# Kernel tuning notes

Measured on AMD Instinct MI355X. Metric: run time of the kernel, lower is better.

The kernel has to match this reference:

```python
import jax, jax.numpy as jnp
import numpy as np

VOCAB = 50257
W_DIM = 1024   # embedding / input width (config.n_embd)
H_DIM = 1024   # LSTM hidden size
NUM_CLASSES = 2
B, T = 32, 2048


def setup_inputs() -> dict:
    key = jax.random.key(0)
    ks = jax.random.split(key, 7)
    s = 0.02
    seq = jax.random.randint(ks[0], (B, T), 0, VOCAB)
    emb = jax.random.normal(ks[1], (VOCAB, W_DIM), dtype=jnp.float32) * s
    W_ih = jax.random.normal(ks[2], (4 * H_DIM, W_DIM), dtype=jnp.float32) * s
    W_hh = jax.random.normal(ks[3], (4 * H_DIM, H_DIM), dtype=jnp.float32) * s
    b_ih = jax.random.normal(ks[4], (4 * H_DIM,), dtype=jnp.float32) * s
    b_hh = jax.random.normal(ks[5], (4 * H_DIM,), dtype=jnp.float32) * s
    W_score = jax.random.normal(ks[6], (NUM_CLASSES, H_DIM), dtype=jnp.float32) * s
    return {"seq": seq, "emb": emb, "W_ih": W_ih, "W_hh": W_hh,
            "b_ih": b_ih, "b_hh": b_hh, "W_score": W_score}


def _lstm_scan(x_gates, W_hh):
    # x_gates: [T, B, 4H] = precomputed input contribution + biases
    H = W_hh.shape[1]
    h0 = jnp.zeros((x_gates.shape[1], H), dtype=x_gates.dtype)
    c0 = jnp.zeros_like(h0)

    def step(carry, xg):
        h, c = carry
        gates = xg + h @ W_hh.T                 # [B, 4H]
        i, f, g, o = jnp.split(gates, 4, axis=-1)  # PyTorch LSTMCell gate order
        i = jax.nn.sigmoid(i)
        f = jax.nn.sigmoid(f)
        g = jnp.tanh(g)
        o = jax.nn.sigmoid(o)
        c = f * c + i * g
        h = o * jnp.tanh(c)
        return (h, c), h

    _, hs = jax.lax.scan(step, (h0, c0), x_gates)  # hs: [T, B, H]
    return hs


def reference(seq, emb, W_ih, W_hh, b_ih, b_hh, W_score):
    # fudge=True: return per-timestep logits [B, T, num_classes]. Dropout in eval mode (identity).
    x = emb[seq]                                      # [B, T, W]
    x_gates = jnp.einsum('btw,gw->btg', x, W_ih) + b_ih + b_hh  # [B, T, 4H]
    hs = _lstm_scan(x_gates.transpose(1, 0, 2), W_hh)           # [T, B, H]
    h = hs.transpose(1, 0, 2)                         # [B, T, H]
    out = jnp.maximum(h, 0.0) @ W_score.T             # score_net: ReLU -> Linear(no bias)
    return out
```

## Files before the change

### kernel.cpp

```cpp
#include <hip/hip_runtime.h>
#include <hip/hip_bf16.h>


typedef _Float16 f16;
typedef _Float16 f16x8 __attribute__((ext_vector_type(8)));
typedef _Float16 f16x4 __attribute__((ext_vector_type(4)));
typedef float    f32x4 __attribute__((ext_vector_type(4)));
typedef unsigned long long u64;

#define B_    32
#define T_    2048
#define H_    1024
#define G4_   4096

__device__ __forceinline__ void gl_lds16(const void* g, void* l) {
  __builtin_amdgcn_global_load_lds(
      (const __attribute__((address_space(1))) void*)g,
      (__attribute__((address_space(3))) void*)l, 16, 0, 0);
}

__device__ __forceinline__ void llc_st64(void* p, u64 v) {
  __hip_atomic_store((u64*)p, v, __ATOMIC_RELAXED, __HIP_MEMORY_SCOPE_AGENT);
}

__device__ __forceinline__ float fast_sigmoid(float v) {
  return __builtin_amdgcn_rcpf(1.f + __expf(-v));
}
__device__ __forceinline__ float fast_tanh(float v) {
  return 1.f - 2.f * __builtin_amdgcn_rcpf(1.f + __expf(2.f * v));
}


__global__ void k_cvt_f16(const float* __restrict__ in, f16* __restrict__ out, long n4) {
  long i = (long)blockIdx.x * blockDim.x + threadIdx.x;
  if (i >= n4) return;
  float4 v = ((const float4*)in)[i];
  f16x4 o; o[0] = (f16)v.x; o[1] = (f16)v.y; o[2] = (f16)v.z; o[3] = (f16)v.w;
  *(f16x4*)(out + i * 4) = o;
}

__global__ void k_whh_reorder(const float* __restrict__ whh, f16* __restrict__ wr) {
  unsigned i = blockIdx.x * blockDim.x + threadIdx.x;
  unsigned e0 = i * 8;
  unsigned R = e0 >> 10, k = e0 & 1023;
  unsigned q = R >> 10, j = R & 1023;
  unsigned outR = ((j >> 4) << 6) + ((j & 15) << 2) + q;
  float4 v0 = ((const float4*)whh)[e0 / 4];
  float4 v1 = ((const float4*)whh)[e0 / 4 + 1];
  f16x8 o;
  o[0] = (f16)v0.x; o[1] = (f16)v0.y; o[2] = (f16)v0.z; o[3] = (f16)v0.w;
  o[4] = (f16)v1.x; o[5] = (f16)v1.y; o[6] = (f16)v1.z; o[7] = (f16)v1.w;
  *(f16x8*)&wr[((size_t)outR << 10) + k] = o;
}

__global__ void k_bias(const float* __restrict__ bi, const float* __restrict__ bh,
                       float* __restrict__ bo) {
  unsigned i = blockIdx.x * blockDim.x + threadIdx.x;
  if (i < G4_) bo[i] = bi[i] + bh[i];
}


__global__ __launch_bounds__(256) void k_gemm_xg(
    const int* __restrict__ seq, const f16* __restrict__ emb16,
    const f16* __restrict__ wih16, const float* __restrict__ bias,
    f16* __restrict__ xg) {
  __shared__ f16 As[128 * 64];
  __shared__ f16 Bs[128 * 64];
  const unsigned tid = threadIdx.x;
  const unsigned w = tid >> 6, lane = tid & 63;
  const unsigned bid = blockIdx.x;
  const unsigned tn = bid & 31, tm = bid >> 5;
  const unsigned wm = (w >> 1) * 64, wn = (w & 1) * 64;

  f32x4 zero = {0.f, 0.f, 0.f, 0.f};
  f32x4 acc[4][4];
#pragma unroll
  for (int i = 0; i < 4; ++i)
#pragma unroll
    for (int j = 0; j < 4; ++j) acc[i][j] = zero;

  for (unsigned kk = 0; kk < 16; ++kk) {
    const unsigned k0 = kk * 64;
#pragma unroll
    for (unsigned c = 0; c < 4; ++c) {
      unsigned idx = c * 256 + tid;
      unsigned row = idx >> 3, ch = idx & 7;
      unsigned chs = ch ^ (row & 7);
      unsigned m = tm * 128 + row;
      unsigned t = m >> 5, b = m & 31;
      int e = seq[b * 2048 + t];
      const f16* src = emb16 + ((size_t)e << 10) + k0 + chs * 8;
      gl_lds16(src, (char*)As + c * 4096 + w * 1024);
    }
#pragma unroll
    for (unsigned c = 0; c < 4; ++c) {
      unsigned idx = c * 256 + tid;
      unsigned row = idx >> 3, ch = idx & 7;
      unsigned chs = ch ^ (row & 7);
      unsigned n = tn * 128 + row;
      const f16* src = wih16 + ((size_t)n << 10) + k0 + chs * 8;
      gl_lds16(src, (char*)Bs + c * 4096 + w * 1024);
    }
    __syncthreads();
#pragma unroll
    for (unsigned ks = 0; ks < 2; ++ks) {
      f16x8 af[4], bf[4];
      unsigned kc = ks * 4 + (lane >> 4);
#pragma unroll
      for (unsigned fm = 0; fm < 4; ++fm) {
        unsigned r = wm + fm * 16 + (lane & 15);
        af[fm] = *(const f16x8*)&As[r * 64 + ((kc ^ (r & 7)) << 3)];
      }
#pragma unroll
      for (unsigned fn = 0; fn < 4; ++fn) {
        unsigned r = wn + fn * 16 + (lane & 15);
        bf[fn] = *(const f16x8*)&Bs[r * 64 + ((kc ^ (r & 7)) << 3)];
      }
#pragma unroll
      for (unsigned fm = 0; fm < 4; ++fm)
#pragma unroll
        for (unsigned fn = 0; fn < 4; ++fn)
          acc[fm][fn] = __builtin_amdgcn_mfma_f32_16x16x32_f16(af[fm], bf[fn], acc[fm][fn], 0, 0, 0);
    }
    __syncthreads();
  }
#pragma unroll
  for (unsigned fn = 0; fn < 4; ++fn) {
    unsigned n = tn * 128 + wn + fn * 16 + (lane & 15);
    unsigned q = n >> 10, j = n & 1023;
    unsigned Rp = ((j >> 4) << 6) + ((j & 15) << 2) + q;
    float bv = bias[n];
#pragma unroll
    for (unsigned fm = 0; fm < 4; ++fm) {
#pragma unroll
      for (unsigned rg = 0; rg < 4; ++rg) {
        unsigned m = tm * 128 + wm + fm * 16 + (lane >> 4) * 4 + rg;
        xg[(size_t)m * G4_ + Rp] = (f16)(acc[fm][fn][rg] + bv);
      }
    }
  }
}


__global__ __launch_bounds__(256) void k_lstm(
    const f16* __restrict__ xg, const f16* __restrict__ wr16,
    f16* __restrict__ h_all) {
  __shared__ f16 Wl[64 * 512];
  __shared__ f16 Hl[2][16 * 1024];
  const unsigned tid = threadIdx.x;
  const unsigned nt = tid >> 6, lane = tid & 63;
  const unsigned wid = blockIdx.x;
  const unsigned rl = lane & 15, hi = lane >> 4;

  for (unsigned c = 0; c < 16; ++c) {
    unsigned idx = c * 256 + tid;
    unsigned row = idx >> 6, ch = idx & 63;
    unsigned chs = ch ^ (row & 7);
    const f16* src = wr16 + (((size_t)wid * 64 + row) << 10) + chs * 8;
    gl_lds16(src, (char*)Wl + c * 4096 + nt * 1024);
  }

  const unsigned rWl = nt * 16 + rl;
  f16x8 breg[16];
  {
    const f16* wp = wr16 + (((size_t)wid * 64 + rWl) << 10) + 512 + hi * 8;
#pragma unroll
    for (int j = 0; j < 16; ++j) {
      asm volatile("global_load_dwordx4 %0, %1, off\n\ts_waitcnt vmcnt(0)"
                   : "=v"(breg[j]) : "v"(wp + j * 32) : "memory");
    }
  }
  __syncthreads();

  const unsigned srow = tid >> 4;
  const unsigned scg = (tid & 15) * 8;
  float cA = 0.f, cB = 0.f;

  for (unsigned t = 1; t <= (unsigned)T_; ++t) {
#pragma unroll
    for (int s = 0; s < 2; ++s) {
      const unsigned sb16 = s * 16;
      const unsigned pb = ((t - 1) * 2 + s) & 1;
      f16x4 xv4 = *(const f16x4*)(xg + ((size_t)(t - 1) * B_ + sb16 + rl) * G4_
                                  + wid * 64 + (nt * 4 + hi) * 4);
      const f16* gp = h_all + ((size_t)(t - 1) * B_ + sb16 + srow) * H_ + scg * 8;
      f16x8 st[8];
      while (true) {
#pragma unroll
        for (int j = 0; j < 8; ++j)
          asm volatile("global_load_dwordx4 %0, %1, off sc0 sc1"
                       : "=v"(st[j]) : "v"(gp + j * 8));
        asm volatile("s_waitcnt vmcnt(0)" ::: "memory");
        __builtin_amdgcn_sched_barrier(0);
        bool ok = true;
#pragma unroll
        for (int j = 0; j < 8; ++j) {
          union { f16x8 v; u64 u[2]; } uu; uu.v = st[j];
          ok = ok && (uu.u[0] != ~0ull) && (uu.u[1] != ~0ull);
        }
        if (ok) break;
        __builtin_amdgcn_s_sleep(1);
      }
#pragma unroll
      for (int j = 0; j < 8; ++j) {
        unsigned cc = scg + j;
        unsigned pos = cc ^ (srow & 7) ^ ((cc >> 3) & 7);
        *(f16x8*)&Hl[pb][srow * 1024 + (pos << 3)] = st[j];
      }
      __syncthreads();

      f32x4 acc0 = {0.f, 0.f, 0.f, 0.f};
      f32x4 acc1 = {0.f, 0.f, 0.f, 0.f};
#pragma unroll
      for (unsigned ks = 0; ks < 16; ks += 2) {
        unsigned c0 = ks * 4 + hi, c1 = c0 + 4;
        unsigned p0 = c0 ^ (rl & 7) ^ ((c0 >> 3) & 7);
        unsigned p1 = c1 ^ (rl & 7) ^ ((c1 >> 3) & 7);
        f16x8 h0 = *(const f16x8*)&Hl[pb][rl * 1024 + (p0 << 3)];
        f16x8 h1 = *(const f16x8*)&Hl[pb][rl * 1024 + (p1 << 3)];
        f16x8 w0 = *(const f16x8*)&Wl[rWl * 512 + ((c0 ^ (rWl & 7)) << 3)];
        f16x8 w1 = *(const f16x8*)&Wl[rWl * 512 + ((c1 ^ (rWl & 7)) << 3)];
        acc0 = __builtin_amdgcn_mfma_f32_16x16x32_f16(w0, h0, acc0, 0, 0, 0);
        acc1 = __builtin_amdgcn_mfma_f32_16x16x32_f16(w1, h1, acc1, 0, 0, 0);
      }
#pragma unroll
      for (unsigned ks = 16; ks < 32; ks += 2) {
        unsigned c0 = ks * 4 + hi, c1 = c0 + 4;
        unsigned p0 = c0 ^ (rl & 7) ^ ((c0 >> 3) & 7);
        unsigned p1 = c1 ^ (rl & 7) ^ ((c1 >> 3) & 7);
        f16x8 h0 = *(const f16x8*)&Hl[pb][rl * 1024 + (p0 << 3)];
        f16x8 h1 = *(const f16x8*)&Hl[pb][rl * 1024 + (p1 << 3)];
        acc0 = __builtin_amdgcn_mfma_f32_16x16x32_f16(breg[ks - 16], h0, acc0, 0, 0, 0);
        acc1 = __builtin_amdgcn_mfma_f32_16x16x32_f16(breg[ks - 15], h1, acc1, 0, 0, 0);
      }
      {
        float gi = acc0[0] + acc1[0] + (float)xv4[0];
        float gf = acc0[1] + acc1[1] + (float)xv4[1];
        float gg = acc0[2] + acc1[2] + (float)xv4[2];
        float go = acc0[3] + acc1[3] + (float)xv4[3];
        float i_ = fast_sigmoid(gi);
        float f_ = fast_sigmoid(gf);
        float g_ = fast_tanh(gg);
        float o_ = fast_sigmoid(go);
        float c_ = (s == 0) ? cA : cB;
        c_ = f_ * c_ + i_ * g_;
        if (s == 0) cA = c_; else cB = c_;
        float hv = o_ * fast_tanh(c_);
        float h1v = __shfl(hv, (int)(rl + 16), 64);
        float h2v = __shfl(hv, (int)(rl + 32), 64);
        float h3v = __shfl(hv, (int)(rl + 48), 64);
        if (hi == 0) {
          union { f16 h4[4]; u64 u; } pk;
          pk.h4[0] = (f16)hv;  pk.h4[1] = (f16)h1v;
          pk.h4[2] = (f16)h2v; pk.h4[3] = (f16)h3v;
          llc_st64(h_all + ((size_t)t * B_ + sb16 + rl) * H_ + wid * 16 + nt * 4,
                   pk.u);
        }
      }
    }
  }
}


__global__ __launch_bounds__(256) void k_logits(
    const f16* __restrict__ h_all, const float* __restrict__ wsc,
    float* __restrict__ out) {
  __shared__ float Ws[2048];
  unsigned tid = threadIdx.x;
  for (unsigned i = tid; i < 512; i += 256) ((float4*)Ws)[i] = ((const float4*)wsc)[i];
  __syncthreads();
  unsigned w = tid >> 6, lane = tid & 63;
  unsigned base = blockIdx.x * 64 + w * 16;
  for (unsigned i = 0; i < 16; ++i) {
    unsigned idx = base + i;
    unsigned tt = idx >> 5, b = idx & 31;
    const f16* hp = h_all + ((size_t)(idx + 32)) * H_ + lane * 16;
    f16x8 ha = *(const f16x8*)hp;
    f16x8 hb = *(const f16x8*)(hp + 8);
    float s0 = 0.f, s1 = 0.f;
#pragma unroll
    for (int z = 0; z < 8; ++z) {
      float hv = fmaxf((float)ha[z], 0.f);
      s0 += hv * Ws[lane * 16 + z];
      s1 += hv * Ws[1024 + lane * 16 + z];
    }
#pragma unroll
    for (int z = 0; z < 8; ++z) {
      float hv = fmaxf((float)hb[z], 0.f);
      s0 += hv * Ws[lane * 16 + 8 + z];
      s1 += hv * Ws[1024 + lane * 16 + 8 + z];
    }
#pragma unroll
    for (int off = 32; off; off >>= 1) {
      s0 += __shfl_xor(s0, off, 64);
      s1 += __shfl_xor(s1, off, 64);
    }
    if (lane == 0) {
      out[((size_t)b * T_ + tt) * 2 + 0] = s0;
      out[((size_t)b * T_ + tt) * 2 + 1] = s1;
    }
  }
}


extern "C" void kernel_launch(void* const* d_in, const int* in_sizes, int n_in,
                              void* d_out, int out_size, void* d_ws, size_t ws_size,
                              hipStream_t stream) {
  const int*   seq = (const int*)d_in[0];
  const float* emb = (const float*)d_in[1];
  const float* wih = (const float*)d_in[2];
  const float* whh = (const float*)d_in[3];
  const float* bih = (const float*)d_in[4];
  const float* bhh = (const float*)d_in[5];
  const float* wsc = (const float*)d_in[6];
  float* out = (float*)d_out;
  char* ws = (char*)d_ws;

  const size_t NEED = 790874112ull;
  if (ws_size < NEED) return;

  f16*   emb16 = (f16*)(ws);
  f16*   wih16 = (f16*)(ws + 102926336ull);
  f16*   wr16  = (f16*)(ws + 111314944ull);
  float* bias  = (float*)(ws + 119703552ull);
  f16*   xg    = (f16*)(ws + 119719936ull);
  f16*   h_all = (f16*)(ws + 656590848ull);

  hipMemsetAsync(h_all, 0, (size_t)B_ * H_ * 2, stream);
  hipMemsetAsync((char*)h_all + (size_t)B_ * H_ * 2, 0xFF,
                 (size_t)T_ * B_ * H_ * 2, stream);

  k_cvt_f16<<<50257, 256, 0, stream>>>(emb, emb16, 12865792L);
  k_cvt_f16<<<4096, 256, 0, stream>>>(wih, wih16, 1048576L);
  k_whh_reorder<<<2048, 256, 0, stream>>>(whh, wr16);
  k_bias<<<16, 256, 0, stream>>>(bih, bhh, bias);

  k_gemm_xg<<<16384, 256, 0, stream>>>(seq, emb16, wih16, bias, xg);
  k_lstm<<<64, 256, 0, stream>>>(xg, wr16, h_all);
  k_logits<<<1024, 256, 0, stream>>>(h_all, wsc, out);
}
```

Measured before the change: 12.78 ms.

## Prefetch next step's hidden state and gate inputs during MFMA compute

Software-pipelines the recurrent loop. The next sub-step's h slab and precomputed x-gate values are now loaded into registers right after the MFMA block, so they are in flight while the current gates are being activated. The spin-wait now checks data that has already arrived and only reloads after a sleep if the data is not yet valid. The block barrier is replaced with an explicit lgkmcnt wait plus s_barrier. The risk is that the early poll often sees h not yet written by other blocks, which forces the sleep and reload path and could add latency on the critical serial chain.

```diff
diff --git a/kernel.cpp b/kernel.cpp
--- a/kernel.cpp
+++ b/kernel.cpp
@@ -175,23 +175,32 @@
   const unsigned srow = tid >> 4;
   const unsigned scg = (tid & 15) * 8;
   float cA = 0.f, cB = 0.f;
+  f16x8 st[8];
+  f16x4 xvA, xvB;
+
+  {
+    const f16* gp0 = h_all + ((size_t)srow) * H_ + scg * 8;
+#pragma unroll
+    for (int j = 0; j < 8; ++j)
+      asm volatile("global_load_dwordx4 %0, %1, off sc0 sc1"
+                   : "=v"(st[j]) : "v"(gp0 + j * 8) : "memory");
+    const f16* xp = xg + ((size_t)rl) * G4_ + wid * 64 + (nt * 4 + hi) * 4;
+    asm volatile("global_load_dwordx2 %0, %1, off"
+                 : "=v"(xvA) : "v"(xp) : "memory");
+    if (hi == 0) {
+      llc_st64(h_all + ((size_t)rl) * H_ + wid * 16 + nt * 4, 0ull);
+    }
+  }
 
   for (unsigned t = 1; t <= (unsigned)T_; ++t) {
 #pragma unroll
     for (int s = 0; s < 2; ++s) {
       const unsigned sb16 = s * 16;
       const unsigned pb = ((t - 1) * 2 + s) & 1;
-      f16x4 xv4 = *(const f16x4*)(xg + ((size_t)(t - 1) * B_ + sb16 + rl) * G4_
-                                  + wid * 64 + (nt * 4 + hi) * 4);
       const f16* gp = h_all + ((size_t)(t - 1) * B_ + sb16 + srow) * H_ + scg * 8;
-      f16x8 st[8];
+      asm volatile("s_waitcnt vmcnt(2)" ::: "memory");
+      __builtin_amdgcn_sched_barrier(0);
       while (true) {
-#pragma unroll
-        for (int j = 0; j < 8; ++j)
-          asm volatile("global_load_dwordx4 %0, %1, off sc0 sc1"
-                       : "=v"(st[j]) : "v"(gp + j * 8));
-        asm volatile("s_waitcnt vmcnt(0)" ::: "memory");
-        __builtin_amdgcn_sched_barrier(0);
         bool ok = true;
 #pragma unroll
         for (int j = 0; j < 8; ++j) {
@@ -200,6 +209,12 @@
         }
         if (ok) break;
         __builtin_amdgcn_s_sleep(1);
+#pragma unroll
+        for (int j = 0; j < 8; ++j)
+          asm volatile("global_load_dwordx4 %0, %1, off sc0 sc1"
+                       : "=v"(st[j]) : "v"(gp + j * 8) : "memory");
+        asm volatile("s_waitcnt vmcnt(0)" ::: "memory");
+        __builtin_amdgcn_sched_barrier(0);
       }
 #pragma unroll
       for (int j = 0; j < 8; ++j) {
@@ -207,7 +222,9 @@
         unsigned pos = cc ^ (srow & 7) ^ ((cc >> 3) & 7);
         *(f16x8*)&Hl[pb][srow * 1024 + (pos << 3)] = st[j];
       }
-      __syncthreads();
+      asm volatile("s_waitcnt lgkmcnt(0)" ::: "memory");
+      __builtin_amdgcn_sched_barrier(0);
+      __builtin_amdgcn_s_barrier();
 
       f32x4 acc0 = {0.f, 0.f, 0.f, 0.f};
       f32x4 acc1 = {0.f, 0.f, 0.f, 0.f};
@@ -233,6 +250,28 @@
         acc0 = __builtin_amdgcn_mfma_f32_16x16x32_f16(breg[ks - 16], h0, acc0, 0, 0, 0);
         acc1 = __builtin_amdgcn_mfma_f32_16x16x32_f16(breg[ks - 15], h1, acc1, 0, 0, 0);
       }
+      asm volatile("s_waitcnt vmcnt(1)" ::: "memory");
+      __builtin_amdgcn_sched_barrier(0);
+      f16x4 xv4 = (s == 0) ? xvA : xvB;
+
+      unsigned nt_t = (s == 0) ? t : (t < (unsigned)T_ ? t + 1 : t);
+      unsigned nsb = (s == 0) ? 16u : 0u;
+      const f16* gpn = h_all + ((size_t)(nt_t - 1) * B_ + nsb + srow) * H_ + scg * 8;
+#pragma unroll
+      for (int j = 0; j < 8; ++j)
+        asm volatile("global_load_dwordx4 %0, %1, off sc0 sc1"
+                     : "=v"(st[j]) : "v"(gpn + j * 8) : "memory");
+      {
+        const f16* xpn = xg + ((size_t)(nt_t - 1) * B_ + nsb + rl) * G4_
+                         + wid * 64 + (nt * 4 + hi) * 4;
+        if (s == 0)
+          asm volatile("global_load_dwordx2 %0, %1, off"
+                       : "=v"(xvB) : "v"(xpn) : "memory");
+        else
+          asm volatile("global_load_dwordx2 %0, %1, off"
+                       : "=v"(xvA) : "v"(xpn) : "memory");
+      }
+
       {
         float gi = acc0[0] + acc1[0] + (float)xv4[0];
         float gf = acc0[1] + acc1[1] + (float)xv4[1];
```

Measured after the change: 11.47 ms (median of 2 runs). -10.2%, faster.
